# Optimization experiments

Measured on AMD Instinct MI355X. Metric: run time of the kernel, lower is better.

The kernel has to match this reference:

```python
import jax, jax.numpy as jnp
import numpy as np

EPS_RMS = 1e-8
EPS_Q = 1e-5


def rms_norm(x, scale):
    # full RMSNorm (p=-1): rms = ||x||_2 / sqrt(d); y = scale * x / (rms + eps)
    d = x.shape[-1]
    norm = jnp.linalg.norm(x, axis=-1, keepdims=True)
    rms = norm * (d ** -0.5)
    return scale * (x / (rms + EPS_RMS))


def activation_quant(x):
    # per-token int8 abs-max quant
    s = 127.0 / jnp.clip(jnp.max(jnp.abs(x), axis=-1, keepdims=True), EPS_Q, None)
    return jnp.clip(jnp.round(x * s), -128, 127) / s


def weight_quant(w):
    # per-tensor ternary abs-mean quant
    s = 1.0 / jnp.clip(jnp.mean(jnp.abs(w)), EPS_Q, None)
    return jnp.clip(jnp.round(w * s), -1, 1) / s


def bit_linear(x, w, scale):
    x_q = activation_quant(rms_norm(x, scale))  # forward value of STE
    w_q = weight_quant(w)
    return x_q @ w_q.T


def setup_inputs() -> dict:
    key = jax.random.key(0)
    ks = jax.random.split(key, 4)
    B = 65536
    x = jax.random.normal(ks[0], (B, 784), dtype=jnp.float32)
    w1 = jax.random.normal(ks[1], (128, 784), dtype=jnp.float32) * (784 ** -0.5)
    w2 = jax.random.normal(ks[2], (64, 128), dtype=jnp.float32) * (128 ** -0.5)
    w3 = jax.random.normal(ks[3], (10, 64), dtype=jnp.float32) * (64 ** -0.5)
    return {
        'x': x,
        'w1': w1, 'scale1': jnp.ones((784,), jnp.float32),
        'w2': w2, 'scale2': jnp.ones((128,), jnp.float32),
        'w3': w3, 'scale3': jnp.ones((64,), jnp.float32),
    }


def reference(x, w1, scale1, w2, scale2, w3, scale3):
    h = jax.nn.relu(bit_linear(x, w1, scale1))
    h = jax.nn.relu(bit_linear(h, w2, scale2))
    return bit_linear(h, w3, scale3)
```

## Files before the change

kernel.cpp:

```cpp
#include <hip/hip_runtime.h>
#include <stdint.h>


typedef int   ix4 __attribute__((ext_vector_type(4)));
typedef float fx4 __attribute__((ext_vector_type(4)));

#define MFMA_I8(a, b, c) __builtin_amdgcn_mfma_i32_16x16x64_i8((a), (b), (c), 0, 0, 0)

__device__ __forceinline__ void sync_lds() {
  asm volatile("s_waitcnt lgkmcnt(0)" ::: "memory");
  __builtin_amdgcn_s_barrier();
}

__global__ __launch_bounds__(256) void prep_mean(
    const float* __restrict__ w1, const float* __restrict__ w2,
    const float* __restrict__ w3, double* __restrict__ sums) {
  __shared__ double red[256];
  const int b = blockIdx.x;
  const float* w; int n, nb, bb, which;
  if (b < 240)      { w = w1; n = 128 * 784; nb = 240; bb = b;       which = 0; }
  else if (b < 248) { w = w2; n = 64 * 128;  nb = 8;   bb = b - 240; which = 1; }
  else              { w = w3; n = 10 * 64;   nb = 1;   bb = 0;       which = 2; }
  double s = 0.0;
  for (int i = bb * 256 + (int)threadIdx.x; i < n; i += nb * 256)
    s += (double)fabsf(w[i]);
  red[threadIdx.x] = s;
  __syncthreads();
  for (int off = 128; off > 0; off >>= 1) {
    if ((int)threadIdx.x < off) red[threadIdx.x] += red[threadIdx.x + off];
    __syncthreads();
  }
  if (threadIdx.x == 0) atomicAdd(&sums[which], red[0]);
}

__global__ __launch_bounds__(256) void prep_quant(
    const float* __restrict__ w1, const float* __restrict__ w2,
    const float* __restrict__ w3, const double* __restrict__ sums,
    int8_t* __restrict__ t1, int8_t* __restrict__ t2,
    int8_t* __restrict__ t3) {
  const int idx = blockIdx.x * 256 + (int)threadIdx.x;
  const float s1 = 1.0f / fmaxf((float)(sums[0] * (1.0 / (128.0 * 784.0))), 1e-5f);
  const float s2 = 1.0f / fmaxf((float)(sums[1] * (1.0 / (64.0 * 128.0))), 1e-5f);
  const float s3 = 1.0f / fmaxf((float)(sums[2] * (1.0 / (10.0 * 64.0))), 1e-5f);
  if (idx < 128 * 832) {
    const int n = idx / 832, k = idx - n * 832;
    float v = 0.f;
    if (k < 784) v = fminf(fmaxf(rintf(w1[n * 784 + k] * s1), -1.f), 1.f);
    t1[idx] = (int8_t)(int)v;
  } else if (idx < 128 * 832 + 64 * 128) {
    const int i = idx - 128 * 832;
    t2[i] = (int8_t)(int)fminf(fmaxf(rintf(w2[i] * s2), -1.f), 1.f);
  } else if (idx < 128 * 832 + 64 * 128 + 16 * 64) {
    const int i = idx - (128 * 832 + 64 * 128);
    const int n = i >> 6, k = i & 63;
    float v = 0.f;
    if (n < 10) v = fminf(fmaxf(rintf(w3[n * 64 + k] * s3), -1.f), 1.f);
    t3[i] = (int8_t)(int)v;
  }
}

__global__ __launch_bounds__(256)
__attribute__((amdgpu_waves_per_eu(2, 4)))
void ffn_main(
    const float* __restrict__ x,
    const float* __restrict__ sc1, const float* __restrict__ sc2,
    const float* __restrict__ sc3,
    const int8_t* __restrict__ t1, const int8_t* __restrict__ t2,
    const int8_t* __restrict__ t3,
    const double* __restrict__ sums,
    float* __restrict__ out, int numTiles) {
  __shared__ int8_t q1[16 * 848];
  __shared__ float  h1[16 * 132];
  __shared__ int8_t q2[16 * 144];
  __shared__ float  h2[16 * 68];
  __shared__ int8_t q3[16 * 80];
  __shared__ float  inv1[16], inv2[16], inv3[16];

  const int tid = threadIdx.x;
  const int l   = tid & 63;
  const int wv  = tid >> 6;
  const int g   = l >> 4;
  const int sl  = l & 15;
  const int token = wv * 4 + g;

  const float m1 = fmaxf((float)(sums[0] * (1.0 / (128.0 * 784.0))), 1e-5f);
  const float m2 = fmaxf((float)(sums[1] * (1.0 / (64.0 * 128.0))), 1e-5f);
  const float m3 = fmaxf((float)(sums[2] * (1.0 / (10.0 * 64.0))), 1e-5f);

  if (tid < 192) {
    const int t = tid / 12, c = tid - (tid / 12) * 12;
    *reinterpret_cast<unsigned*>(&q1[t * 848 + 784 + c * 4]) = 0u;
  }

  fx4 xv[13];
  int tile = blockIdx.x;
  if (tile < numTiles) {
    const float* rowp = x + (size_t)(tile * 16 + token) * 784;
#pragma unroll
    for (int c = 0; c < 12; ++c)
      xv[c] = *reinterpret_cast<const fx4*>(rowp + (sl + 16 * c) * 4);
    if (sl < 4) xv[12] = *reinterpret_cast<const fx4*>(rowp + (sl + 192) * 4);
  }

  for (; tile < numTiles; tile += (int)gridDim.x) {
    float ss = 0.f, am = 0.f;
#pragma unroll
    for (int c = 0; c < 12; ++c) {
      fx4 v = xv[c];
      fx4 s4 = *reinterpret_cast<const fx4*>(sc1 + (sl + 16 * c) * 4);
      ss += v[0] * v[0] + v[1] * v[1] + v[2] * v[2] + v[3] * v[3];
      am = fmaxf(am, fmaxf(fmaxf(fabsf(v[0] * s4[0]), fabsf(v[1] * s4[1])),
                           fmaxf(fabsf(v[2] * s4[2]), fabsf(v[3] * s4[3]))));
    }
    if (sl < 4) {
      fx4 v = xv[12];
      fx4 s4 = *reinterpret_cast<const fx4*>(sc1 + (sl + 192) * 4);
      ss += v[0] * v[0] + v[1] * v[1] + v[2] * v[2] + v[3] * v[3];
      am = fmaxf(am, fmaxf(fmaxf(fabsf(v[0] * s4[0]), fabsf(v[1] * s4[1])),
                           fmaxf(fabsf(v[2] * s4[2]), fabsf(v[3] * s4[3]))));
    }
#pragma unroll
    for (int m = 1; m < 16; m <<= 1) {
      ss += __shfl_xor(ss, m, 64);
      am = fmaxf(am, __shfl_xor(am, m, 64));
    }
    const float denom = sqrtf(ss) * (1.0f / 28.0f) + 1e-8f;
    const float invd  = 1.0f / denom;
    const float cl    = fmaxf(am * invd, 1e-5f);
    const float gq    = (127.0f / cl) * invd;
    if (sl == 0) inv1[token] = cl * (1.0f / 127.0f);

#pragma unroll
    for (int c = 0; c < 12; ++c) {
      fx4 v = xv[c];
      fx4 s4 = *reinterpret_cast<const fx4*>(sc1 + (sl + 16 * c) * 4);
      int q0 = (int)fminf(fmaxf(rintf(v[0] * s4[0] * gq), -128.f), 127.f);
      int q1i = (int)fminf(fmaxf(rintf(v[1] * s4[1] * gq), -128.f), 127.f);
      int q2i = (int)fminf(fmaxf(rintf(v[2] * s4[2] * gq), -128.f), 127.f);
      int q3i = (int)fminf(fmaxf(rintf(v[3] * s4[3] * gq), -128.f), 127.f);
      unsigned p = (unsigned)(q0 & 255) | ((unsigned)(q1i & 255) << 8) |
                   ((unsigned)(q2i & 255) << 16) | ((unsigned)(q3i & 255) << 24);
      *reinterpret_cast<unsigned*>(&q1[token * 848 + (sl + 16 * c) * 4]) = p;
    }
    if (sl < 4) {
      fx4 v = xv[12];
      fx4 s4 = *reinterpret_cast<const fx4*>(sc1 + (sl + 192) * 4);
      int q0 = (int)fminf(fmaxf(rintf(v[0] * s4[0] * gq), -128.f), 127.f);
      int q1i = (int)fminf(fmaxf(rintf(v[1] * s4[1] * gq), -128.f), 127.f);
      int q2i = (int)fminf(fmaxf(rintf(v[2] * s4[2] * gq), -128.f), 127.f);
      int q3i = (int)fminf(fmaxf(rintf(v[3] * s4[3] * gq), -128.f), 127.f);
      unsigned p = (unsigned)(q0 & 255) | ((unsigned)(q1i & 255) << 8) |
                   ((unsigned)(q2i & 255) << 16) | ((unsigned)(q3i & 255) << 24);
      *reinterpret_cast<unsigned*>(&q1[token * 848 + (sl + 192) * 4]) = p;
    }

    {
      const int ntile = tile + (int)gridDim.x;
      if (ntile < numTiles) {
        const float* rowp = x + (size_t)(ntile * 16 + token) * 784;
#pragma unroll
        for (int c = 0; c < 12; ++c)
          xv[c] = *reinterpret_cast<const fx4*>(rowp + (sl + 16 * c) * 4);
        if (sl < 4) xv[12] = *reinterpret_cast<const fx4*>(rowp + (sl + 192) * 4);
      }
    }

    sync_lds();

    ix4 acc0 = {0, 0, 0, 0}, acc1 = {0, 0, 0, 0};
    {
      const int8_t* b0p = t1 + (wv * 32 + sl) * 832;
      const int8_t* b1p = b0p + 16 * 832;
#pragma unroll 4
      for (int kk = 0; kk < 13; ++kk) {
        const int k0 = kk * 64 + g * 16;
        ix4 a  = *reinterpret_cast<const ix4*>(&q1[sl * 848 + k0]);
        ix4 b0 = *reinterpret_cast<const ix4*>(b0p + k0);
        ix4 b1 = *reinterpret_cast<const ix4*>(b1p + k0);
        acc0 = MFMA_I8(a, b0, acc0);
        acc1 = MFMA_I8(a, b1, acc1);
      }
    }
#pragma unroll
    for (int r = 0; r < 4; ++r) {
      const int tr = g * 4 + r;
      const float s = inv1[tr] * m1;
      h1[tr * 132 + wv * 32 + sl]      = fmaxf((float)acc0[r] * s, 0.f);
      h1[tr * 132 + wv * 32 + 16 + sl] = fmaxf((float)acc1[r] * s, 0.f);
    }
    sync_lds();

    {
      fx4 v0 = *reinterpret_cast<const fx4*>(&h1[token * 132 + sl * 4]);
      fx4 v1 = *reinterpret_cast<const fx4*>(&h1[token * 132 + 64 + sl * 4]);
      fx4 s0 = *reinterpret_cast<const fx4*>(sc2 + sl * 4);
      fx4 s1 = *reinterpret_cast<const fx4*>(sc2 + 64 + sl * 4);
      float ss2 = v0[0]*v0[0] + v0[1]*v0[1] + v0[2]*v0[2] + v0[3]*v0[3]
                + v1[0]*v1[0] + v1[1]*v1[1] + v1[2]*v1[2] + v1[3]*v1[3];
      float am2 = fmaxf(fmaxf(fmaxf(fabsf(v0[0]*s0[0]), fabsf(v0[1]*s0[1])),
                              fmaxf(fabsf(v0[2]*s0[2]), fabsf(v0[3]*s0[3]))),
                        fmaxf(fmaxf(fabsf(v1[0]*s1[0]), fabsf(v1[1]*s1[1])),
                              fmaxf(fabsf(v1[2]*s1[2]), fabsf(v1[3]*s1[3]))));
#pragma unroll
      for (int m = 1; m < 16; m <<= 1) {
        ss2 += __shfl_xor(ss2, m, 64);
        am2 = fmaxf(am2, __shfl_xor(am2, m, 64));
      }
      const float den2 = sqrtf(ss2) * 0.08838834764831845f + 1e-8f;
      const float id2  = 1.0f / den2;
      const float cl2  = fmaxf(am2 * id2, 1e-5f);
      const float gq2  = (127.0f / cl2) * id2;
      if (sl == 0) inv2[token] = cl2 * (1.0f / 127.0f);
      int a0 = (int)fminf(fmaxf(rintf(v0[0]*s0[0]*gq2), -128.f), 127.f);
      int a1 = (int)fminf(fmaxf(rintf(v0[1]*s0[1]*gq2), -128.f), 127.f);
      int a2 = (int)fminf(fmaxf(rintf(v0[2]*s0[2]*gq2), -128.f), 127.f);
      int a3 = (int)fminf(fmaxf(rintf(v0[3]*s0[3]*gq2), -128.f), 127.f);
      int b0 = (int)fminf(fmaxf(rintf(v1[0]*s1[0]*gq2), -128.f), 127.f);
      int b1 = (int)fminf(fmaxf(rintf(v1[1]*s1[1]*gq2), -128.f), 127.f);
      int b2 = (int)fminf(fmaxf(rintf(v1[2]*s1[2]*gq2), -128.f), 127.f);
      int b3 = (int)fminf(fmaxf(rintf(v1[3]*s1[3]*gq2), -128.f), 127.f);
      unsigned pa = (unsigned)(a0 & 255) | ((unsigned)(a1 & 255) << 8) |
                    ((unsigned)(a2 & 255) << 16) | ((unsigned)(a3 & 255) << 24);
      unsigned pb = (unsigned)(b0 & 255) | ((unsigned)(b1 & 255) << 8) |
                    ((unsigned)(b2 & 255) << 16) | ((unsigned)(b3 & 255) << 24);
      *reinterpret_cast<unsigned*>(&q2[token * 144 + sl * 4]) = pa;
      *reinterpret_cast<unsigned*>(&q2[token * 144 + 64 + sl * 4]) = pb;
    }
    sync_lds();

    ix4 acc2 = {0, 0, 0, 0};
    {
      const int8_t* bp = t2 + (wv * 16 + sl) * 128;
#pragma unroll
      for (int kk = 0; kk < 2; ++kk) {
        const int k0 = kk * 64 + g * 16;
        ix4 a = *reinterpret_cast<const ix4*>(&q2[sl * 144 + k0]);
        ix4 b = *reinterpret_cast<const ix4*>(bp + k0);
        acc2 = MFMA_I8(a, b, acc2);
      }
    }
#pragma unroll
    for (int r = 0; r < 4; ++r) {
      const int tr = g * 4 + r;
      h2[tr * 68 + wv * 16 + sl] = fmaxf((float)acc2[r] * inv2[tr] * m2, 0.f);
    }
    sync_lds();

    {
      fx4 v = *reinterpret_cast<const fx4*>(&h2[token * 68 + sl * 4]);
      fx4 s = *reinterpret_cast<const fx4*>(sc3 + sl * 4);
      float ss3 = v[0]*v[0] + v[1]*v[1] + v[2]*v[2] + v[3]*v[3];
      float am3 = fmaxf(fmaxf(fabsf(v[0]*s[0]), fabsf(v[1]*s[1])),
                        fmaxf(fabsf(v[2]*s[2]), fabsf(v[3]*s[3])));
#pragma unroll
      for (int m = 1; m < 16; m <<= 1) {
        ss3 += __shfl_xor(ss3, m, 64);
        am3 = fmaxf(am3, __shfl_xor(am3, m, 64));
      }
      const float den3 = sqrtf(ss3) * 0.125f + 1e-8f;
      const float id3  = 1.0f / den3;
      const float cl3  = fmaxf(am3 * id3, 1e-5f);
      const float gq3  = (127.0f / cl3) * id3;
      if (sl == 0) inv3[token] = cl3 * (1.0f / 127.0f);
      int c0 = (int)fminf(fmaxf(rintf(v[0]*s[0]*gq3), -128.f), 127.f);
      int c1 = (int)fminf(fmaxf(rintf(v[1]*s[1]*gq3), -128.f), 127.f);
      int c2 = (int)fminf(fmaxf(rintf(v[2]*s[2]*gq3), -128.f), 127.f);
      int c3 = (int)fminf(fmaxf(rintf(v[3]*s[3]*gq3), -128.f), 127.f);
      unsigned p = (unsigned)(c0 & 255) | ((unsigned)(c1 & 255) << 8) |
                   ((unsigned)(c2 & 255) << 16) | ((unsigned)(c3 & 255) << 24);
      *reinterpret_cast<unsigned*>(&q3[token * 80 + sl * 4]) = p;
    }
    sync_lds();

    if (wv == 0) {
      ix4 acc3 = {0, 0, 0, 0};
      ix4 a = *reinterpret_cast<const ix4*>(&q3[sl * 80 + g * 16]);
      ix4 b = *reinterpret_cast<const ix4*>(t3 + sl * 64 + g * 16);
      acc3 = MFMA_I8(a, b, acc3);
      if (sl < 10) {
        const long tok0 = (long)tile * 16;
#pragma unroll
        for (int r = 0; r < 4; ++r) {
          const int tr = g * 4 + r;
          out[(tok0 + tr) * 10 + sl] = (float)acc3[r] * inv3[tr] * m3;
        }
      }
    }
    sync_lds();
  }
}

extern "C" void kernel_launch(void* const* d_in, const int* in_sizes, int n_in,
                              void* d_out, int out_size, void* d_ws, size_t ws_size,
                              hipStream_t stream) {
  const float* x  = (const float*)d_in[0];
  const float* w1 = (const float*)d_in[1];
  const float* s1 = (const float*)d_in[2];
  const float* w2 = (const float*)d_in[3];
  const float* s2 = (const float*)d_in[4];
  const float* w3 = (const float*)d_in[5];
  const float* s3 = (const float*)d_in[6];
  float* out = (float*)d_out;

  char* ws = (char*)d_ws;
  double* sums = (double*)ws;
  int8_t* t1 = (int8_t*)(ws + 256);
  int8_t* t2 = (int8_t*)(ws + 106752);
  int8_t* t3 = (int8_t*)(ws + 114944);

  const int B = in_sizes[0] / 784;
  const int numTiles = B / 16;

  hipMemsetAsync(sums, 0, 3 * sizeof(double), stream);
  prep_mean<<<249, 256, 0, stream>>>(w1, w2, w3, sums);
  const int total_q = 128 * 832 + 64 * 128 + 16 * 64;
  prep_quant<<<(total_q + 255) / 256, 256, 0, stream>>>(w1, w2, w3, sums, t1, t2, t3);
  const int grid = numTiles < 1024 ? numTiles : 1024;
  ffn_main<<<grid, 256, 0, stream>>>(x, s1, s2, s3, t1, t2, t3, sums, out, numTiles);
}
```

Measured before the change: 319.8 us.

## Split layers 2-3 into a separate register-resident kernel via global int8 staging

```diff
diff --git a/kernel.cpp b/kernel.cpp
--- a/kernel.cpp
+++ b/kernel.cpp
@@ -10,6 +10,9 @@
 __device__ __forceinline__ void sync_lds() {
   asm volatile("s_waitcnt lgkmcnt(0)" ::: "memory");
   __builtin_amdgcn_s_barrier();
+}
+__device__ __forceinline__ void wave_lds_fence() {
+  asm volatile("s_waitcnt lgkmcnt(0)" ::: "memory");
 }
 
 __global__ __launch_bounds__(256) void prep_mean(
@@ -37,7 +40,7 @@
     const float* __restrict__ w1, const float* __restrict__ w2,
     const float* __restrict__ w3, const double* __restrict__ sums,
     int8_t* __restrict__ t1, int8_t* __restrict__ t2,
-    int8_t* __restrict__ t3) {
+    int8_t* __restrict__ t3p) {
   const int idx = blockIdx.x * 256 + (int)threadIdx.x;
   const float s1 = 1.0f / fmaxf((float)(sums[0] * (1.0 / (128.0 * 784.0))), 1e-5f);
   const float s2 = 1.0f / fmaxf((float)(sums[1] * (1.0 / (64.0 * 128.0))), 1e-5f);
@@ -52,29 +55,24 @@
     t2[i] = (int8_t)(int)fminf(fmaxf(rintf(w2[i] * s2), -1.f), 1.f);
   } else if (idx < 128 * 832 + 64 * 128 + 16 * 64) {
     const int i = idx - (128 * 832 + 64 * 128);
-    const int n = i >> 6, k = i & 63;
+    const int n = i >> 6, p = i & 63;
+    const int ch = (p >> 2) + 16 * (p & 3);
     float v = 0.f;
-    if (n < 10) v = fminf(fmaxf(rintf(w3[n * 64 + k] * s3), -1.f), 1.f);
-    t3[i] = (int8_t)(int)v;
+    if (n < 10) v = fminf(fmaxf(rintf(w3[n * 64 + ch] * s3), -1.f), 1.f);
+    t3p[i] = (int8_t)(int)v;
   }
 }
 
 __global__ __launch_bounds__(256)
 __attribute__((amdgpu_waves_per_eu(2, 4)))
-void ffn_main(
+void ffn_l1(
     const float* __restrict__ x,
     const float* __restrict__ sc1, const float* __restrict__ sc2,
-    const float* __restrict__ sc3,
-    const int8_t* __restrict__ t1, const int8_t* __restrict__ t2,
-    const int8_t* __restrict__ t3,
-    const double* __restrict__ sums,
-    float* __restrict__ out, int numTiles) {
+    const int8_t* __restrict__ t1, const double* __restrict__ sums,
+    int8_t* __restrict__ q2g, float* __restrict__ inv2g, int numTiles) {
   __shared__ int8_t q1[16 * 848];
   __shared__ float  h1[16 * 132];
-  __shared__ int8_t q2[16 * 144];
-  __shared__ float  h2[16 * 68];
-  __shared__ int8_t q3[16 * 80];
-  __shared__ float  inv1[16], inv2[16], inv3[16];
+  __shared__ float  inv1[16];
 
   const int tid = threadIdx.x;
   const int l   = tid & 63;
@@ -84,8 +82,6 @@
   const int token = wv * 4 + g;
 
   const float m1 = fmaxf((float)(sums[0] * (1.0 / (128.0 * 784.0))), 1e-5f);
-  const float m2 = fmaxf((float)(sums[1] * (1.0 / (64.0 * 128.0))), 1e-5f);
-  const float m3 = fmaxf((float)(sums[2] * (1.0 / (10.0 * 64.0))), 1e-5f);
 
   if (tid < 192) {
     const int t = tid / 12, c = tid - (tid / 12) * 12;
@@ -210,7 +206,8 @@
       const float id2  = 1.0f / den2;
       const float cl2  = fmaxf(am2 * id2, 1e-5f);
       const float gq2  = (127.0f / cl2) * id2;
-      if (sl == 0) inv2[token] = cl2 * (1.0f / 127.0f);
+      const size_t tok = (size_t)tile * 16 + token;
+      if (sl == 0) inv2g[tok] = cl2 * (1.0f / 127.0f);
       int a0 = (int)fminf(fmaxf(rintf(v0[0]*s0[0]*gq2), -128.f), 127.f);
       int a1 = (int)fminf(fmaxf(rintf(v0[1]*s0[1]*gq2), -128.f), 127.f);
       int a2 = (int)fminf(fmaxf(rintf(v0[2]*s0[2]*gq2), -128.f), 127.f);
@@ -223,70 +220,97 @@
                     ((unsigned)(a2 & 255) << 16) | ((unsigned)(a3 & 255) << 24);
       unsigned pb = (unsigned)(b0 & 255) | ((unsigned)(b1 & 255) << 8) |
                     ((unsigned)(b2 & 255) << 16) | ((unsigned)(b3 & 255) << 24);
-      *reinterpret_cast<unsigned*>(&q2[token * 144 + sl * 4]) = pa;
-      *reinterpret_cast<unsigned*>(&q2[token * 144 + 64 + sl * 4]) = pb;
-    }
-    sync_lds();
-
-    ix4 acc2 = {0, 0, 0, 0};
-    {
-      const int8_t* bp = t2 + (wv * 16 + sl) * 128;
-#pragma unroll
-      for (int kk = 0; kk < 2; ++kk) {
-        const int k0 = kk * 64 + g * 16;
-        ix4 a = *reinterpret_cast<const ix4*>(&q2[sl * 144 + k0]);
-        ix4 b = *reinterpret_cast<const ix4*>(bp + k0);
-        acc2 = MFMA_I8(a, b, acc2);
-      }
-    }
+      *reinterpret_cast<unsigned*>(q2g + tok * 128 + sl * 4)      = pa;
+      *reinterpret_cast<unsigned*>(q2g + tok * 128 + 64 + sl * 4) = pb;
+    }
+  }
+}
+
+__global__ __launch_bounds__(256) void ffn_l23(
+    const int8_t* __restrict__ q2g, const float* __restrict__ inv2g,
+    const float* __restrict__ sc3,
+    const int8_t* __restrict__ t2, const int8_t* __restrict__ t3p,
+    const double* __restrict__ sums, float* __restrict__ out) {
+  __shared__ int8_t wbuf[4][16 * 64];
+
+  const int tid = threadIdx.x;
+  const int l   = tid & 63;
+  const int wv  = tid >> 6;
+  const int g   = l >> 4;
+  const int sl  = l & 15;
+  const int wtok0 = (blockIdx.x * 4 + wv) * 16;
+
+  const float m2 = fmaxf((float)(sums[1] * (1.0 / (64.0 * 128.0))), 1e-5f);
+  const float m3 = fmaxf((float)(sums[2] * (1.0 / (10.0 * 64.0))), 1e-5f);
+
+  ix4 a0 = *reinterpret_cast<const ix4*>(q2g + (size_t)(wtok0 + sl) * 128 + g * 16);
+  ix4 a1 = *reinterpret_cast<const ix4*>(q2g + (size_t)(wtok0 + sl) * 128 + 64 + g * 16);
+  fx4 i2 = *reinterpret_cast<const fx4*>(inv2g + wtok0 + 4 * g);
+
+  ix4 acc[4];
+#pragma unroll
+  for (int nt = 0; nt < 4; ++nt) {
+    ix4 c = {0, 0, 0, 0};
+    const int8_t* bp = t2 + (nt * 16 + sl) * 128;
+    c = MFMA_I8(a0, *reinterpret_cast<const ix4*>(bp + g * 16), c);
+    c = MFMA_I8(a1, *reinterpret_cast<const ix4*>(bp + 64 + g * 16), c);
+    acc[nt] = c;
+  }
+
+  float sc3v[4];
+#pragma unroll
+  for (int nt = 0; nt < 4; ++nt) sc3v[nt] = sc3[nt * 16 + sl];
+
+  float h2v[4][4];
+  float ss3[4] = {0.f, 0.f, 0.f, 0.f}, am3[4] = {0.f, 0.f, 0.f, 0.f};
+#pragma unroll
+  for (int nt = 0; nt < 4; ++nt)
 #pragma unroll
     for (int r = 0; r < 4; ++r) {
-      const int tr = g * 4 + r;
-      h2[tr * 68 + wv * 16 + sl] = fmaxf((float)acc2[r] * inv2[tr] * m2, 0.f);
-    }
-    sync_lds();
-
-    {
-      fx4 v = *reinterpret_cast<const fx4*>(&h2[token * 68 + sl * 4]);
-      fx4 s = *reinterpret_cast<const fx4*>(sc3 + sl * 4);
-      float ss3 = v[0]*v[0] + v[1]*v[1] + v[2]*v[2] + v[3]*v[3];
-      float am3 = fmaxf(fmaxf(fabsf(v[0]*s[0]), fabsf(v[1]*s[1])),
-                        fmaxf(fabsf(v[2]*s[2]), fabsf(v[3]*s[3])));
-#pragma unroll
-      for (int m = 1; m < 16; m <<= 1) {
-        ss3 += __shfl_xor(ss3, m, 64);
-        am3 = fmaxf(am3, __shfl_xor(am3, m, 64));
-      }
-      const float den3 = sqrtf(ss3) * 0.125f + 1e-8f;
-      const float id3  = 1.0f / den3;
-      const float cl3  = fmaxf(am3 * id3, 1e-5f);
-      const float gq3  = (127.0f / cl3) * id3;
-      if (sl == 0) inv3[token] = cl3 * (1.0f / 127.0f);
-      int c0 = (int)fminf(fmaxf(rintf(v[0]*s[0]*gq3), -128.f), 127.f);
-      int c1 = (int)fminf(fmaxf(rintf(v[1]*s[1]*gq3), -128.f), 127.f);
-      int c2 = (int)fminf(fmaxf(rintf(v[2]*s[2]*gq3), -128.f), 127.f);
-      int c3 = (int)fminf(fmaxf(rintf(v[3]*s[3]*gq3), -128.f), 127.f);
-      unsigned p = (unsigned)(c0 & 255) | ((unsigned)(c1 & 255) << 8) |
-                   ((unsigned)(c2 & 255) << 16) | ((unsigned)(c3 & 255) << 24);
-      *reinterpret_cast<unsigned*>(&q3[token * 80 + sl * 4]) = p;
-    }
-    sync_lds();
-
-    if (wv == 0) {
-      ix4 acc3 = {0, 0, 0, 0};
-      ix4 a = *reinterpret_cast<const ix4*>(&q3[sl * 80 + g * 16]);
-      ix4 b = *reinterpret_cast<const ix4*>(t3 + sl * 64 + g * 16);
-      acc3 = MFMA_I8(a, b, acc3);
-      if (sl < 10) {
-        const long tok0 = (long)tile * 16;
-#pragma unroll
-        for (int r = 0; r < 4; ++r) {
-          const int tr = g * 4 + r;
-          out[(tok0 + tr) * 10 + sl] = (float)acc3[r] * inv3[tr] * m3;
-        }
-      }
-    }
-    sync_lds();
+      float h = fmaxf((float)acc[nt][r] * i2[r] * m2, 0.f);
+      h2v[nt][r] = h;
+      ss3[r] += h * h;
+      am3[r] = fmaxf(am3[r], fabsf(h * sc3v[nt]));
+    }
+#pragma unroll
+  for (int m = 1; m < 16; m <<= 1) {
+#pragma unroll
+    for (int r = 0; r < 4; ++r) {
+      ss3[r] += __shfl_xor(ss3[r], m, 64);
+      am3[r] = fmaxf(am3[r], __shfl_xor(am3[r], m, 64));
+    }
+  }
+  float gq3[4], i3[4];
+#pragma unroll
+  for (int r = 0; r < 4; ++r) {
+    const float den3 = sqrtf(ss3[r]) * 0.125f + 1e-8f;
+    const float id3  = 1.0f / den3;
+    const float cl3  = fmaxf(am3[r] * id3, 1e-5f);
+    gq3[r] = (127.0f / cl3) * id3;
+    i3[r]  = cl3 * (1.0f / 127.0f) * m3;
+  }
+
+#pragma unroll
+  for (int r = 0; r < 4; ++r) {
+    int c0 = (int)fminf(fmaxf(rintf(h2v[0][r] * sc3v[0] * gq3[r]), -128.f), 127.f);
+    int c1 = (int)fminf(fmaxf(rintf(h2v[1][r] * sc3v[1] * gq3[r]), -128.f), 127.f);
+    int c2 = (int)fminf(fmaxf(rintf(h2v[2][r] * sc3v[2] * gq3[r]), -128.f), 127.f);
+    int c3 = (int)fminf(fmaxf(rintf(h2v[3][r] * sc3v[3] * gq3[r]), -128.f), 127.f);
+    unsigned p = (unsigned)(c0 & 255) | ((unsigned)(c1 & 255) << 8) |
+                 ((unsigned)(c2 & 255) << 16) | ((unsigned)(c3 & 255) << 24);
+    *reinterpret_cast<unsigned*>(&wbuf[wv][(4 * g + r) * 64 + sl * 4]) = p;
+  }
+  wave_lds_fence();
+
+  ix4 a3 = *reinterpret_cast<const ix4*>(&wbuf[wv][sl * 64 + g * 16]);
+  ix4 b3 = *reinterpret_cast<const ix4*>(t3p + sl * 64 + g * 16);
+  ix4 acc3 = {0, 0, 0, 0};
+  acc3 = MFMA_I8(a3, b3, acc3);
+
+  if (sl < 10) {
+#pragma unroll
+    for (int r = 0; r < 4; ++r)
+      out[(size_t)(wtok0 + 4 * g + r) * 10 + sl] = (float)acc3[r] * i3[r];
   }
 }
 
@@ -304,9 +328,11 @@
 
   char* ws = (char*)d_ws;
   double* sums = (double*)ws;
-  int8_t* t1 = (int8_t*)(ws + 256);
-  int8_t* t2 = (int8_t*)(ws + 106752);
-  int8_t* t3 = (int8_t*)(ws + 114944);
+  int8_t* t1   = (int8_t*)(ws + 1024);
+  int8_t* t2   = (int8_t*)(ws + 107520);
+  int8_t* t3p  = (int8_t*)(ws + 115712);
+  float*  inv2 = (float*)(ws + 116736);
+  int8_t* q2   = (int8_t*)(ws + 378880);
 
   const int B = in_sizes[0] / 784;
   const int numTiles = B / 16;
@@ -314,7 +340,8 @@
   hipMemsetAsync(sums, 0, 3 * sizeof(double), stream);
   prep_mean<<<249, 256, 0, stream>>>(w1, w2, w3, sums);
   const int total_q = 128 * 832 + 64 * 128 + 16 * 64;
-  prep_quant<<<(total_q + 255) / 256, 256, 0, stream>>>(w1, w2, w3, sums, t1, t2, t3);
-  const int grid = numTiles < 1024 ? numTiles : 1024;
-  ffn_main<<<grid, 256, 0, stream>>>(x, s1, s2, s3, t1, t2, t3, sums, out, numTiles);
-}
+  prep_quant<<<(total_q + 255) / 256, 256, 0, stream>>>(w1, w2, w3, sums, t1, t2, t3p);
+  const int grid1 = numTiles < 1024 ? numTiles : 1024;
+  ffn_l1<<<grid1, 256, 0, stream>>>(x, s1, s2, t1, sums, q2, inv2, numTiles);
+  ffn_l23<<<B / 64, 256, 0, stream>>>(q2, inv2, s3, t2, t3p, sums, out);
+}
```

Result: no change. 319.5 us (-0.1%).
